# Performance work log

Hardware: AMD Instinct MI355X
Metric: run time of the kernel (lower is better)

## Reference

```python
import jax, jax.numpy as jnp
import numpy as np

LAMBDA_COLOR = 0.01
BLUR = 0.01          # geomloss blur
P = 2                # geomloss p
EPS_FINAL = BLUR ** P  # 1e-4
# Note: with scaling=1.2 (>1), geomloss's epsilon_schedule arange is empty, so
# eps_list = [diameter**p, blur**p] -> exactly two annealing stages.


def cost_matrix(x, y, lambda_color):
    # x: [B,N,6], y: [B,M,6]
    cx, col_x = x[..., :3], x[..., 3:]
    cy, col_y = y[..., :3], y[..., 3:]
    max_norm = jnp.max(jnp.linalg.norm(jnp.concatenate([cx, cy], axis=1), axis=-1))
    s = 1.0 / (max_norm + 1e-6)
    cxn, cyn = cx * s, cy * s
    coord = jnp.sum((cxn[:, :, None, :] - cyn[:, None, :, :]) ** 2, axis=-1)  # [B,N,M]
    col_x = jnp.clip(col_x, 0.0, 1.0)
    col_y = jnp.clip(col_y, 0.0, 1.0)
    col = jnp.sum((col_x[:, :, None, :] - col_y[:, None, :, :]) ** 2, axis=-1)
    return jnp.maximum(coord + lambda_color * col, 0.0)


def softmin(eps, C, h):
    # h: [B,M] = log_weights + potential/eps ; C: [B,N,M]
    return -eps * jax.nn.logsumexp(h[:, None, :] - C / eps, axis=2)  # [B,N]


def sinkhorn_distance(x, y, lambda_color):
    B, N, _ = x.shape
    M = y.shape[1]
    a_log = jnp.full((B, N), -np.log(N), dtype=x.dtype)
    b_log = jnp.full((B, M), -np.log(M), dtype=x.dtype)

    C_xy = cost_matrix(x, y, lambda_color)          # [B,N,M]
    C_yx = jnp.swapaxes(C_xy, 1, 2)                 # cost is symmetric in x<->y

    # diameter over raw 6-d features (geomloss max_diameter)
    pts = jnp.concatenate([x.reshape(-1, x.shape[-1]), y.reshape(-1, y.shape[-1])], axis=0)
    diameter = jnp.linalg.norm(pts.max(0) - pts.min(0))
    eps_list = (diameter ** P, jnp.asarray(EPS_FINAL, x.dtype))

    # Sinkhorn loop runs without gradient through the potentials (geomloss semantics)
    Cs_xy = jax.lax.stop_gradient(C_xy)
    Cs_yx = jax.lax.stop_gradient(C_yx)

    eps = eps_list[0]
    f = softmin(eps, Cs_xy, b_log)   # potential on x
    g = softmin(eps, Cs_yx, a_log)   # potential on y
    for eps in eps_list:
        ft = softmin(eps, Cs_xy, b_log + g / eps)
        gt = softmin(eps, Cs_yx, a_log + f / eps)
        f, g = 0.5 * (f + ft), 0.5 * (g + gt)

    # final extrapolation with gradient-carrying cost, detached dual potentials
    eps = eps_list[-1]
    f_new = softmin(eps, C_xy, b_log + jax.lax.stop_gradient(g) / eps)
    g_new = softmin(eps, C_yx, a_log + jax.lax.stop_gradient(f) / eps)

    # <a,f> + <b,g> with uniform weights
    ot = f_new.mean(axis=1) + g_new.mean(axis=1)   # [B]
    return ot.mean() * 10.0


def setup_inputs() -> dict:
    key = jax.random.key(0)
    kx, ky = jax.random.split(key)
    x = jax.random.normal(kx, (4, 4096, 6), dtype=jnp.float32)
    y = jax.random.normal(ky, (4, 4096, 6), dtype=jnp.float32)
    return {"x": x, "y": y}


def reference(x, y):
    return sinkhorn_distance(x, y, LAMBDA_COLOR)
```

## Files before the change

### kernel.cpp

```cpp
#include <hip/hip_runtime.h>

#define ROWS 16384
#define PTS_TOTAL 32768
#define NSM_BLK 256

#define LOG2E 1.4426950408889634f
#define LN2   0.6931471805599453f
#define NEG_LOG2M (-12.0f)
#define EPS1LNM 8.317766166719343e-4f

typedef _Float16 h2 __attribute__((ext_vector_type(2)));
typedef _Float16 v8h __attribute__((ext_vector_type(8)));
typedef float f32x4 __attribute__((ext_vector_type(4)));

__device__ inline float fexp2(float x) { return __builtin_amdgcn_exp2f(x); }
__device__ inline float flog2(float x) { return __builtin_amdgcn_logf(x); }

__device__ inline unsigned fenc(float f) {
  unsigned u = __float_as_uint(f);
  return (u & 0x80000000u) ? ~u : (u | 0x80000000u);
}
__device__ inline float fdec(unsigned u) {
  return (u & 0x80000000u) ? __uint_as_float(u & 0x7fffffffu)
                           : __uint_as_float(~u);
}
__device__ inline unsigned pkh2(float a, float b) {
  h2 hv; hv.x = (_Float16)a; hv.y = (_Float16)b;
  return __builtin_bit_cast(unsigned, hv);
}
__device__ inline v8h bcv8(uint4 u) { return __builtin_bit_cast(v8h, u); }

__device__ inline float mkv(const float* __restrict__ p, float s, float* v) {
  v[0] = p[0] * s; v[1] = p[1] * s; v[2] = p[2] * s;
  v[3] = 0.1f * fminf(fmaxf(p[3], 0.0f), 1.0f);
  v[4] = 0.1f * fminf(fmaxf(p[4], 0.0f), 1.0f);
  v[5] = 0.1f * fminf(fmaxf(p[5], 0.0f), 1.0f);
  return v[0]*v[0] + v[1]*v[1] + v[2]*v[2] + v[3]*v[3] + v[4]*v[4] + v[5]*v[5];
}

__device__ inline float taylor_f(const float* __restrict__ M, const float* v,
                                 float q, float eps0) {
  float sc2 = 2.0f * LOG2E / eps0;
  float p[6];
#pragma unroll
  for (int d = 0; d < 6; ++d) p[d] = v[d] * sc2;
  float t1 = 0.0f;
#pragma unroll
  for (int d = 0; d < 6; ++d) t1 += p[d] * M[1 + d];
  float t2 = 0.0f;
  int kk = 7;
#pragma unroll
  for (int d = 0; d < 6; ++d) {
#pragma unroll
    for (int e = d; e < 6; ++e) {
      float coef = (d == e) ? 1.0f : 2.0f;
      t2 += coef * p[d] * p[e] * M[kk];
      kk++;
    }
  }
  float S = M[0] + LN2 * t1 + (0.5f * LN2 * LN2) * t2;
  return q - eps0 * LN2 * flog2(S);
}

__device__ inline void mom28(float* acc, float wgt, const float* v) {
  acc[0] = wgt;
  int kk = 1;
#pragma unroll
  for (int d = 0; d < 6; ++d) acc[kk++] = wgt * v[d];
#pragma unroll
  for (int d = 0; d < 6; ++d) {
    float wv = wgt * v[d];
#pragma unroll
    for (int e = d; e < 6; ++e) acc[kk++] = wv * v[e];
  }
}

__device__ inline void red28g(float* acc, float* __restrict__ dst,
                              float (*shf)[28], int t, int wave, int lane) {
#pragma unroll
  for (int off = 32; off > 0; off >>= 1) {
#pragma unroll
    for (int k = 0; k < 28; ++k) acc[k] += __shfl_xor(acc[k], off);
  }
  if (lane == 0) {
#pragma unroll
    for (int k = 0; k < 28; ++k) shf[wave][k] = acc[k];
  }
  __syncthreads();
  if (t < 28) dst[t] = (shf[0][t] + shf[1][t]) + (shf[2][t] + shf[3][t]);
}

__device__ inline void se_from_rmax(const unsigned* __restrict__ RMAXu,
                                    unsigned (*shu)[13], float& s, float& eps0,
                                    int t, int wave, int lane) {
  int set = t & 127;
  unsigned e[13];
#pragma unroll
  for (int k = 0; k < 13; ++k) e[k] = RMAXu[set * 16 + k];
#pragma unroll
  for (int off = 32; off > 0; off >>= 1) {
#pragma unroll
    for (int k = 0; k < 13; ++k) {
      unsigned o = (unsigned)__shfl_xor((int)e[k], off);
      e[k] = e[k] > o ? e[k] : o;
    }
  }
  if (lane == 0) {
#pragma unroll
    for (int k = 0; k < 13; ++k) shu[wave][k] = e[k];
  }
  __syncthreads();
  unsigned mm[13];
#pragma unroll
  for (int k = 0; k < 13; ++k) {
    unsigned v0 = shu[0][k] > shu[1][k] ? shu[0][k] : shu[1][k];
    unsigned v1 = shu[2][k] > shu[3][k] ? shu[2][k] : shu[3][k];
    mm[k] = v0 > v1 ? v0 : v1;
  }
  s = 1.0f / (sqrtf(fdec(mm[0])) + 1e-6f);
  eps0 = 0.0f;
#pragma unroll
  for (int k = 0; k < 6; ++k) {
    float dd = fdec(mm[1 + k]) + fdec(mm[7 + k]);
    eps0 += dd * dd;
  }
}

__global__ __launch_bounds__(256) void k1_max(
    const float* __restrict__ x, const float* __restrict__ y,
    float* __restrict__ w) {
  unsigned* BARC = (unsigned*)w;
  unsigned* RMAX = (unsigned*)w + 64;
  const int t = threadIdx.x, wave = t >> 6, lane = t & 63, bx = blockIdx.x;
  if (bx == 0 && t == 0) BARC[0] = 0u;
  const int g0 = bx * 256;
  bool isx = g0 < ROWS;
  __shared__ float4 st[384];
  const float4* src =
      (const float4*)((isx ? x : y) + (size_t)(g0 & (ROWS - 1)) * 6);
  st[t] = src[t];
  if (t < 128) st[256 + t] = src[256 + t];
  __syncthreads();
  const float* sp = (const float*)st + t * 6;
  float d[6];
#pragma unroll
  for (int k = 0; k < 6; ++k) d[k] = sp[k];
  unsigned e[13];
  e[0] = fenc(d[0] * d[0] + d[1] * d[1] + d[2] * d[2]);
#pragma unroll
  for (int k = 0; k < 6; ++k) {
    e[1 + k] = fenc(d[k]);
    e[7 + k] = fenc(-d[k]);
  }
#pragma unroll
  for (int off = 32; off > 0; off >>= 1) {
#pragma unroll
    for (int k = 0; k < 13; ++k) {
      unsigned o = (unsigned)__shfl_xor((int)e[k], off);
      e[k] = e[k] > o ? e[k] : o;
    }
  }
  __shared__ unsigned shu[4][13];
  if (lane == 0) {
#pragma unroll
    for (int k = 0; k < 13; ++k) shu[wave][k] = e[k];
  }
  __syncthreads();
  if (t < 13) {
    unsigned v = shu[0][t];
#pragma unroll
    for (int wv = 1; wv < 4; ++wv) v = v > shu[wv][t] ? v : shu[wv][t];
    RMAX[bx * 16 + t] = v;
  }
}

__global__ __launch_bounds__(256) void k2_pack(
    const float* __restrict__ x, const float* __restrict__ y,
    float* __restrict__ w) {
  const int t = threadIdx.x, wave = t >> 6, lane = t & 63, bx = blockIdx.x;
  const unsigned* RMAX = (const unsigned*)w + 64;
  float* MOMP1 = w + 2560;
  float* base = w + 16384;
  uint4* AREC = (uint4*)base;
  float* Qarr = base + 3 * 4 * PTS_TOTAL;

  __shared__ unsigned shu[4][13];
  __shared__ float shf[4][28];
  float s, eps0;
  se_from_rmax(RMAX, shu, s, eps0, t, wave, lane);

  const int g = bx * 256 + t;
  const int side = g >> 14;
  const float* p = (side ? y : x) + (size_t)(g & (ROWS - 1)) * 6;
  float v[6]; float q = mkv(p, s, v);
  Qarr[g] = q;
  unsigned w01 = pkh2(v[0], v[1]), w23 = pkh2(v[2], v[3]), w45 = pkh2(v[4], v[5]);
  AREC[g] = (uint4){w01, w23, w45, pkh2(1.0f, 0.0f)};

  float wgt = fexp2(NEG_LOG2M - q * (LOG2E / eps0));
  float acc[28];
  mom28(acc, wgt, v);
  red28g(acc, MOMP1 + (size_t)bx * 32, shf, t, wave, lane);
}

__global__ __launch_bounds__(256) void k3_rows1(
    const float* __restrict__ x, const float* __restrict__ y,
    float* __restrict__ w) {
  const int t = threadIdx.x, wave = t >> 6, lane = t & 63, bx = blockIdx.x;
  const unsigned* RMAX = (const unsigned*)w + 64;
  const float* MOMP1 = w + 2560;
  float* MOMP2 = w + 2560 + 4096;
  float* base = w + 16384;
  float* FG1 = base + 3 * 4 * PTS_TOTAL + PTS_TOTAL + PTS_TOTAL;

  __shared__ unsigned shu[4][13];
  __shared__ float shf[4][28];
  __shared__ float M1opp[28];
  float s, eps0;
  se_from_rmax(RMAX, shu, s, eps0, t, wave, lane);

  const int g = bx * 256 + t;
  const int side = g >> 14;
  const int batch = (g >> 12) & 3;
  if (t < 28) {
    const float* mp = MOMP1 + ((size_t)((side ^ 1) * 64 + batch * 16)) * 32 + t;
    float m = 0.0f;
#pragma unroll
    for (int j = 0; j < 16; ++j) m += mp[j * 32];
    M1opp[t] = m;
  }
  __syncthreads();

  const float* p = (side ? y : x) + (size_t)(g & (ROWS - 1)) * 6;
  float v[6]; float q = mkv(p, s, v);
  float f1 = taylor_f(M1opp, v, q, eps0);
  FG1[g] = f1;
  float w2 = fexp2(NEG_LOG2M + (f1 - q) * (LOG2E / eps0));
  float acc[28];
  mom28(acc, w2, v);
  red28g(acc, MOMP2 + (size_t)bx * 32, shf, t, wave, lane);
}

__global__ __launch_bounds__(256) void k4_rows2(
    const float* __restrict__ x, const float* __restrict__ y,
    float* __restrict__ w) {
  const int t = threadIdx.x, wave = t >> 6, lane = t & 63, bx = blockIdx.x;
  const unsigned* RMAX = (const unsigned*)w + 64;
  const float* MOMP2 = w + 2560 + 4096;
  float* base = w + 16384;
  uint4* BRECA = (uint4*)base + PTS_TOTAL;
  float* Qarr = base + 3 * 4 * PTS_TOTAL;
  float* FG2 = Qarr + PTS_TOTAL;
  const float* FG1 = FG2 + PTS_TOTAL;

  __shared__ unsigned shu[4][13];
  __shared__ float M2opp[28];
  float s, eps0;
  se_from_rmax(RMAX, shu, s, eps0, t, wave, lane);

  const int g = bx * 256 + t;
  const int side = g >> 14;
  const int batch = (g >> 12) & 3;
  if (t < 28) {
    const float* mp = MOMP2 + ((size_t)((side ^ 1) * 64 + batch * 16)) * 32 + t;
    float m = 0.0f;
#pragma unroll
    for (int j = 0; j < 16; ++j) m += mp[j * 32];
    M2opp[t] = m;
  }
  __syncthreads();

  const float* p = (side ? y : x) + (size_t)(g & (ROWS - 1)) * 6;
  float v[6]; float q = mkv(p, s, v);
  float f1 = FG1[g];
  float f_t = taylor_f(M2opp, v, q, eps0);
  float f2 = 0.5f * (f1 + f_t);
  FG2[g] = f2;
  float hs2 = 0.5f * (f2 - q - EPS1LNM);
  unsigned w01 = pkh2(v[0], v[1]), w23 = pkh2(v[2], v[3]), w45 = pkh2(v[4], v[5]);
  BRECA[g] = (uint4){w01, w23, w45, pkh2(hs2, 0.0f)};
}

__device__ inline int xcd_rowgrp(int bx) {
  return (bx & 7) * 32 + (bx >> 3);
}

__device__ inline float softmax_max128L(int grow0,
                                        const uint4* __restrict__ AREC,
                                        const uint4* __restrict__ BIN,
                                        uint4* __restrict__ Blds,
                                        float (*lm)[64]) {
  int t = threadIdx.x;
  int w = t >> 6, lane = t & 63;
  int l16 = lane & 15;
  bool ldq = lane < 16;
  int side = grow0 >> 14;
  int batch = (grow0 & (ROWS - 1)) >> 12;
  int panel0 = (side ^ 1) * ROWS + batch * 4096;

  const uint4* gsrc = BIN + panel0 + w * 512 + lane;
  uint4* ldst = Blds + w * 512 + lane;
  uint4 s0 = gsrc[0],   s1 = gsrc[64],  s2 = gsrc[128], s3 = gsrc[192];
  uint4 s4 = gsrc[256], s5 = gsrc[320], s6 = gsrc[384], s7 = gsrc[448];

  uint4 z4 = (uint4){0u, 0u, 0u, 0u};
  uint4 a0u = z4, a1u = z4, a2u = z4, a3u = z4;
  int arow = grow0 + (w >> 2) * 64;
  if (ldq) {
    a0u = AREC[arow + l16];
    a1u = AREC[arow + 16 + l16];
    a2u = AREC[arow + 32 + l16];
    a3u = AREC[arow + 48 + l16];
  }
  v8h a0 = bcv8(a0u), a1 = bcv8(a1u), a2 = bcv8(a2u), a3 = bcv8(a3u);

  ldst[0] = s0;   ldst[64] = s1;  ldst[128] = s2; ldst[192] = s3;
  ldst[256] = s4; ldst[320] = s5; ldst[384] = s6; ldst[448] = s7;
  __syncthreads();

  f32x4 m0 = {-3.0e38f, -3.0e38f, -3.0e38f, -3.0e38f};
  f32x4 m1 = m0, m2 = m0, m3 = m0;
  const f32x4 cz = {0.0f, 0.0f, 0.0f, 0.0f};
  const int colq = (w & 3) * 1024;

#pragma unroll 8
  for (int tt = 0; tt < 64; ++tt) {
    uint4 bu = z4;
    if (ldq) bu = Blds[colq + tt * 16 + l16];
    v8h b = bcv8(bu);
    f32x4 d0 = __builtin_amdgcn_mfma_f32_16x16x32_f16(a0, b, cz, 0, 0, 0);
    f32x4 d1 = __builtin_amdgcn_mfma_f32_16x16x32_f16(a1, b, cz, 0, 0, 0);
    f32x4 d2 = __builtin_amdgcn_mfma_f32_16x16x32_f16(a2, b, cz, 0, 0, 0);
    f32x4 d3 = __builtin_amdgcn_mfma_f32_16x16x32_f16(a3, b, cz, 0, 0, 0);
    m0 = __builtin_elementwise_max(m0, d0);
    m1 = __builtin_elementwise_max(m1, d1);
    m2 = __builtin_elementwise_max(m2, d2);
    m3 = __builtin_elementwise_max(m3, d3);
  }

#pragma unroll
  for (int off = 1; off <= 8; off <<= 1) {
#pragma unroll
    for (int r = 0; r < 4; ++r) {
      m0[r] = fmaxf(m0[r], __shfl_xor(m0[r], off));
      m1[r] = fmaxf(m1[r], __shfl_xor(m1[r], off));
      m2[r] = fmaxf(m2[r], __shfl_xor(m2[r], off));
      m3[r] = fmaxf(m3[r], __shfl_xor(m3[r], off));
    }
  }
  if (l16 == 0) {
    int qd = lane >> 4;
#pragma unroll
    for (int r = 0; r < 4; ++r) {
      lm[w][qd * 4 + r]      = m0[r];
      lm[w][16 + qd * 4 + r] = m1[r];
      lm[w][32 + qd * 4 + r] = m2[r];
      lm[w][48 + qd * 4 + r] = m3[r];
    }
  }
  __syncthreads();
  float m = 0.0f;
  if (t < 128) {
    int half4 = (t >> 6) * 4, lr = t & 63;
    m = fmaxf(fmaxf(lm[half4][lr], lm[half4 + 1][lr]),
              fmaxf(lm[half4 + 2][lr], lm[half4 + 3][lr]));
  }
  return m;
}

__global__ __launch_bounds__(512) void kb_sm1(
    const uint4* __restrict__ AREC, const uint4* __restrict__ BIN,
    uint4* __restrict__ BOUT, const float* __restrict__ Qarr,
    const float* __restrict__ FG2) {
  __shared__ uint4 Blds[4096];
  __shared__ float lm[8][64];
  int t = threadIdx.x;
  int grow0 = xcd_rowgrp(blockIdx.x) * 128;
  float qv = 0.0f, fprev = 0.0f;
  uint4 ar = (uint4){0u, 0u, 0u, 0u};
  if (t < 128) {
    int gg = grow0 + t;
    qv = Qarr[gg];
    fprev = FG2[gg];
    ar = AREC[gg];
  }
  float m = softmax_max128L(grow0, AREC, BIN, Blds, lm);
  if (t < 128) {
    float f_t = qv - 2.0f * m;
    float fo = 0.5f * (fprev + f_t);
    float hs = 0.5f * (fo - qv - EPS1LNM);
    BOUT[grow0 + t] = (uint4){ar.x, ar.y, ar.z, pkh2(hs, 0.0f)};
  }
}

__global__ __launch_bounds__(512) void kc_sm2(
    const uint4* __restrict__ AREC, const uint4* __restrict__ BIN,
    const float* __restrict__ Qarr, float* __restrict__ PART,
    unsigned* __restrict__ BARC, float* __restrict__ out) {
  __shared__ uint4 Blds[4096];
  __shared__ float lm[8][64];
  __shared__ float fsh[128];
  __shared__ float fred[8];
  __shared__ int lastf;
  int t = threadIdx.x;
  int wave = t >> 6, lane = t & 63;
  int grow0 = xcd_rowgrp(blockIdx.x) * 128;
  float qv = 0.0f;
  if (t < 128) qv = Qarr[grow0 + t];
  float m = softmax_max128L(grow0, AREC, BIN, Blds, lm);
  if (t < 128) fsh[t] = qv - 2.0f * m;
  __syncthreads();
  if (t == 0) {
    float ssum = 0.0f;
#pragma unroll
    for (int k = 0; k < 128; ++k) ssum += fsh[k];
    __hip_atomic_store(&PART[blockIdx.x], ssum, __ATOMIC_RELAXED,
                       __HIP_MEMORY_SCOPE_AGENT);
    unsigned old = __hip_atomic_fetch_add(BARC, 1u, __ATOMIC_ACQ_REL,
                                          __HIP_MEMORY_SCOPE_AGENT);
    lastf = (old == (unsigned)(NSM_BLK - 1)) ? 1 : 0;
  }
  __syncthreads();
  if (lastf) {
    float a = 0.0f;
    if (t < NSM_BLK)
      a = __hip_atomic_load(&PART[t], __ATOMIC_RELAXED,
                            __HIP_MEMORY_SCOPE_AGENT);
#pragma unroll
    for (int off = 32; off > 0; off >>= 1) a += __shfl_xor(a, off);
    if (lane == 0) fred[wave] = a;
    __syncthreads();
    if (t == 0) {
      float s8 = 0.0f;
#pragma unroll
      for (int k = 0; k < 8; ++k) s8 += fred[k];
      out[0] = s8 * (10.0f / (float)ROWS);
    }
  }
}

extern "C" void kernel_launch(void* const* d_in, const int* in_sizes, int n_in,
                              void* d_out, int out_size, void* d_ws,
                              size_t ws_size, hipStream_t stream) {
  const float* x = (const float*)d_in[0];
  const float* y = (const float*)d_in[1];
  float* out = (float*)d_out;
  float* w = (float*)d_ws;

  unsigned* BARC = (unsigned*)w;
  float* base = w + 16384;
  uint4* AREC  = (uint4*)base;
  uint4* BRECA = AREC + PTS_TOTAL;
  uint4* BRECB = BRECA + PTS_TOTAL;
  float* Qarr  = base + 3 * 4 * PTS_TOTAL;
  float* FG2   = Qarr + PTS_TOTAL;
  float* FG1   = FG2 + PTS_TOTAL;
  float* PART  = FG1 + PTS_TOTAL;

  (void)ws_size;
  k1_max<<<128, 256, 0, stream>>>(x, y, w);
  k2_pack<<<128, 256, 0, stream>>>(x, y, w);
  k3_rows1<<<128, 256, 0, stream>>>(x, y, w);
  k4_rows2<<<128, 256, 0, stream>>>(x, y, w);
  kb_sm1<<<NSM_BLK, 512, 0, stream>>>(AREC, BRECA, BRECB, Qarr, FG2);
  kc_sm2<<<NSM_BLK, 512, 0, stream>>>(AREC, BRECB, Qarr, PART, BARC, out);
}
```

Baseline: 97.81 us.

## Repartition softmin max so each wave covers all rows over its own column slice

Each wave now computes MFMA row maxima for all 128 rows against only the 512 columns it staged itself, instead of 64 rows against 1024 shared columns. Because a wave reads only LDS it wrote, the block-wide barrier after staging is replaced by a wave-local lgkmcnt wait. This halves LDS B reads per MFMA and removes a barrier, at the cost of holding eight A fragments and eight max accumulators per wave (more registers) and a larger cross-wave reduction buffer.

Measured after the change: 98.72 us. Within noise of the previous version (+0.9%).

```diff
diff --git a/kernel.cpp b/kernel.cpp
--- a/kernel.cpp
+++ b/kernel.cpp
@@ -285,11 +285,11 @@
   return (bx & 7) * 32 + (bx >> 3);
 }
 
-__device__ inline float softmax_max128L(int grow0,
-                                        const uint4* __restrict__ AREC,
-                                        const uint4* __restrict__ BIN,
-                                        uint4* __restrict__ Blds,
-                                        float (*lm)[64]) {
+__device__ inline float softmax_wp128(int grow0,
+                                      const uint4* __restrict__ AREC,
+                                      const uint4* __restrict__ BIN,
+                                      uint4* __restrict__ Blds,
+                                      float (*lm)[128]) {
   int t = threadIdx.x;
   int w = t >> 6, lane = t & 63;
   int l16 = lane & 15;
@@ -305,28 +305,29 @@
 
   uint4 z4 = (uint4){0u, 0u, 0u, 0u};
   uint4 a0u = z4, a1u = z4, a2u = z4, a3u = z4;
-  int arow = grow0 + (w >> 2) * 64;
+  uint4 a4u = z4, a5u = z4, a6u = z4, a7u = z4;
   if (ldq) {
-    a0u = AREC[arow + l16];
-    a1u = AREC[arow + 16 + l16];
-    a2u = AREC[arow + 32 + l16];
-    a3u = AREC[arow + 48 + l16];
+    a0u = AREC[grow0 + l16];        a1u = AREC[grow0 + 16 + l16];
+    a2u = AREC[grow0 + 32 + l16];   a3u = AREC[grow0 + 48 + l16];
+    a4u = AREC[grow0 + 64 + l16];   a5u = AREC[grow0 + 80 + l16];
+    a6u = AREC[grow0 + 96 + l16];   a7u = AREC[grow0 + 112 + l16];
   }
   v8h a0 = bcv8(a0u), a1 = bcv8(a1u), a2 = bcv8(a2u), a3 = bcv8(a3u);
+  v8h a4 = bcv8(a4u), a5 = bcv8(a5u), a6 = bcv8(a6u), a7 = bcv8(a7u);
 
   ldst[0] = s0;   ldst[64] = s1;  ldst[128] = s2; ldst[192] = s3;
   ldst[256] = s4; ldst[320] = s5; ldst[384] = s6; ldst[448] = s7;
-  __syncthreads();
+  asm volatile("s_waitcnt lgkmcnt(0)" ::: "memory");
 
   f32x4 m0 = {-3.0e38f, -3.0e38f, -3.0e38f, -3.0e38f};
-  f32x4 m1 = m0, m2 = m0, m3 = m0;
+  f32x4 m1 = m0, m2 = m0, m3 = m0, m4 = m0, m5 = m0, m6 = m0, m7 = m0;
   const f32x4 cz = {0.0f, 0.0f, 0.0f, 0.0f};
-  const int colq = (w & 3) * 1024;
-
-#pragma unroll 8
-  for (int tt = 0; tt < 64; ++tt) {
+  const int col0 = w * 512;
+
+#pragma unroll 4
+  for (int tt = 0; tt < 32; ++tt) {
     uint4 bu = z4;
-    if (ldq) bu = Blds[colq + tt * 16 + l16];
+    if (ldq) bu = Blds[col0 + tt * 16 + l16];
     v8h b = bcv8(bu);
     f32x4 d0 = __builtin_amdgcn_mfma_f32_16x16x32_f16(a0, b, cz, 0, 0, 0);
     f32x4 d1 = __builtin_amdgcn_mfma_f32_16x16x32_f16(a1, b, cz, 0, 0, 0);
@@ -336,6 +337,14 @@
     m1 = __builtin_elementwise_max(m1, d1);
     m2 = __builtin_elementwise_max(m2, d2);
     m3 = __builtin_elementwise_max(m3, d3);
+    f32x4 d4 = __builtin_amdgcn_mfma_f32_16x16x32_f16(a4, b, cz, 0, 0, 0);
+    f32x4 d5 = __builtin_amdgcn_mfma_f32_16x16x32_f16(a5, b, cz, 0, 0, 0);
+    f32x4 d6 = __builtin_amdgcn_mfma_f32_16x16x32_f16(a6, b, cz, 0, 0, 0);
+    f32x4 d7 = __builtin_amdgcn_mfma_f32_16x16x32_f16(a7, b, cz, 0, 0, 0);
+    m4 = __builtin_elementwise_max(m4, d4);
+    m5 = __builtin_elementwise_max(m5, d5);
+    m6 = __builtin_elementwise_max(m6, d6);
+    m7 = __builtin_elementwise_max(m7, d7);
   }
 
 #pragma unroll
@@ -346,24 +355,32 @@
       m1[r] = fmaxf(m1[r], __shfl_xor(m1[r], off));
       m2[r] = fmaxf(m2[r], __shfl_xor(m2[r], off));
       m3[r] = fmaxf(m3[r], __shfl_xor(m3[r], off));
+      m4[r] = fmaxf(m4[r], __shfl_xor(m4[r], off));
+      m5[r] = fmaxf(m5[r], __shfl_xor(m5[r], off));
+      m6[r] = fmaxf(m6[r], __shfl_xor(m6[r], off));
+      m7[r] = fmaxf(m7[r], __shfl_xor(m7[r], off));
     }
   }
   if (l16 == 0) {
     int qd = lane >> 4;
 #pragma unroll
     for (int r = 0; r < 4; ++r) {
-      lm[w][qd * 4 + r]      = m0[r];
-      lm[w][16 + qd * 4 + r] = m1[r];
-      lm[w][32 + qd * 4 + r] = m2[r];
-      lm[w][48 + qd * 4 + r] = m3[r];
+      lm[w][qd * 4 + r]       = m0[r];
+      lm[w][16 + qd * 4 + r]  = m1[r];
+      lm[w][32 + qd * 4 + r]  = m2[r];
+      lm[w][48 + qd * 4 + r]  = m3[r];
+      lm[w][64 + qd * 4 + r]  = m4[r];
+      lm[w][80 + qd * 4 + r]  = m5[r];
+      lm[w][96 + qd * 4 + r]  = m6[r];
+      lm[w][112 + qd * 4 + r] = m7[r];
     }
   }
   __syncthreads();
   float m = 0.0f;
   if (t < 128) {
-    int half4 = (t >> 6) * 4, lr = t & 63;
-    m = fmaxf(fmaxf(lm[half4][lr], lm[half4 + 1][lr]),
-              fmaxf(lm[half4 + 2][lr], lm[half4 + 3][lr]));
+    float ma = fmaxf(fmaxf(lm[0][t], lm[1][t]), fmaxf(lm[2][t], lm[3][t]));
+    float mb = fmaxf(fmaxf(lm[4][t], lm[5][t]), fmaxf(lm[6][t], lm[7][t]));
+    m = fmaxf(ma, mb);
   }
   return m;
 }
@@ -373,7 +390,7 @@
     uint4* __restrict__ BOUT, const float* __restrict__ Qarr,
     const float* __restrict__ FG2) {
   __shared__ uint4 Blds[4096];
-  __shared__ float lm[8][64];
+  __shared__ float lm[8][128];
   int t = threadIdx.x;
   int grow0 = xcd_rowgrp(blockIdx.x) * 128;
   float qv = 0.0f, fprev = 0.0f;
@@ -384,7 +401,7 @@
     fprev = FG2[gg];
     ar = AREC[gg];
   }
-  float m = softmax_max128L(grow0, AREC, BIN, Blds, lm);
+  float m = softmax_wp128(grow0, AREC, BIN, Blds, lm);
   if (t < 128) {
     float f_t = qv - 2.0f * m;
     float fo = 0.5f * (fprev + f_t);
@@ -398,7 +415,7 @@
     const float* __restrict__ Qarr, float* __restrict__ PART,
     unsigned* __restrict__ BARC, float* __restrict__ out) {
   __shared__ uint4 Blds[4096];
-  __shared__ float lm[8][64];
+  __shared__ float lm[8][128];
   __shared__ float fsh[128];
   __shared__ float fred[8];
   __shared__ int lastf;
@@ -407,7 +424,7 @@
   int grow0 = xcd_rowgrp(blockIdx.x) * 128;
   float qv = 0.0f;
   if (t < 128) qv = Qarr[grow0 + t];
-  float m = softmax_max128L(grow0, AREC, BIN, Blds, lm);
+  float m = softmax_wp128(grow0, AREC, BIN, Blds, lm);
   if (t < 128) fsh[t] = qv - 2.0f * m;
   __syncthreads();
   if (t == 0) {
```

## Fuse four prologue kernels into one persistent kernel with grid barriers

Applied to the files above, without the earlier changes.

Replaces the four small prologue kernels (max, pack, first and second Taylor-moment steps) with one 64-block, 512-thread kernel. The stages are separated by atomic-counter grid barriers, and each thread keeps its point data in registers across them. This removes three kernel launch gaps, the redundant global reductions that recomputed scale and eps in every kernel, and the FG1 round-trip through memory. A small init kernel zeroes the barrier counters. It relies on all 64 blocks being co-resident, and it trades launch overhead for spin-wait barrier latency.

Measured after the change: 102.4 us. 1.05x slower.

```diff
diff --git a/kernel.cpp b/kernel.cpp
--- a/kernel.cpp
+++ b/kernel.cpp
@@ -3,6 +3,7 @@
 #define ROWS 16384
 #define PTS_TOTAL 32768
 #define NSM_BLK 256
+#define NEPS_BLK 64
 
 #define LOG2E 1.4426950408889634f
 #define LN2   0.6931471805599453f
@@ -30,11 +31,11 @@
 }
 __device__ inline v8h bcv8(uint4 u) { return __builtin_bit_cast(v8h, u); }
 
-__device__ inline float mkv(const float* __restrict__ p, float s, float* v) {
-  v[0] = p[0] * s; v[1] = p[1] * s; v[2] = p[2] * s;
-  v[3] = 0.1f * fminf(fmaxf(p[3], 0.0f), 1.0f);
-  v[4] = 0.1f * fminf(fmaxf(p[4], 0.0f), 1.0f);
-  v[5] = 0.1f * fminf(fmaxf(p[5], 0.0f), 1.0f);
+__device__ inline float mkv_d(const float* d, float s, float* v) {
+  v[0] = d[0] * s; v[1] = d[1] * s; v[2] = d[2] * s;
+  v[3] = 0.1f * fminf(fmaxf(d[3], 0.0f), 1.0f);
+  v[4] = 0.1f * fminf(fmaxf(d[4], 0.0f), 1.0f);
+  v[5] = 0.1f * fminf(fmaxf(d[5], 0.0f), 1.0f);
   return v[0]*v[0] + v[1]*v[1] + v[2]*v[2] + v[3]*v[3] + v[4]*v[4] + v[5]*v[5];
 }
 
@@ -75,209 +76,189 @@
   }
 }
 
-__device__ inline void red28g(float* acc, float* __restrict__ dst,
-                              float (*shf)[28], int t, int wave, int lane) {
-#pragma unroll
-  for (int off = 32; off > 0; off >>= 1) {
-#pragma unroll
-    for (int k = 0; k < 28; ++k) acc[k] += __shfl_xor(acc[k], off);
-  }
-  if (lane == 0) {
-#pragma unroll
-    for (int k = 0; k < 28; ++k) shf[wave][k] = acc[k];
-  }
-  __syncthreads();
-  if (t < 28) dst[t] = (shf[0][t] + shf[1][t]) + (shf[2][t] + shf[3][t]);
-}
-
-__device__ inline void se_from_rmax(const unsigned* __restrict__ RMAXu,
-                                    unsigned (*shu)[13], float& s, float& eps0,
-                                    int t, int wave, int lane) {
-  int set = t & 127;
-  unsigned e[13];
-#pragma unroll
-  for (int k = 0; k < 13; ++k) e[k] = RMAXu[set * 16 + k];
-#pragma unroll
-  for (int off = 32; off > 0; off >>= 1) {
-#pragma unroll
-    for (int k = 0; k < 13; ++k) {
-      unsigned o = (unsigned)__shfl_xor((int)e[k], off);
-      e[k] = e[k] > o ? e[k] : o;
-    }
-  }
-  if (lane == 0) {
-#pragma unroll
-    for (int k = 0; k < 13; ++k) shu[wave][k] = e[k];
-  }
-  __syncthreads();
-  unsigned mm[13];
-#pragma unroll
-  for (int k = 0; k < 13; ++k) {
-    unsigned v0 = shu[0][k] > shu[1][k] ? shu[0][k] : shu[1][k];
-    unsigned v1 = shu[2][k] > shu[3][k] ? shu[2][k] : shu[3][k];
-    mm[k] = v0 > v1 ? v0 : v1;
-  }
-  s = 1.0f / (sqrtf(fdec(mm[0])) + 1e-6f);
-  eps0 = 0.0f;
-#pragma unroll
-  for (int k = 0; k < 6; ++k) {
-    float dd = fdec(mm[1 + k]) + fdec(mm[7 + k]);
-    eps0 += dd * dd;
-  }
-}
-
-__global__ __launch_bounds__(256) void k1_max(
-    const float* __restrict__ x, const float* __restrict__ y,
-    float* __restrict__ w) {
-  unsigned* BARC = (unsigned*)w;
-  unsigned* RMAX = (unsigned*)w + 64;
-  const int t = threadIdx.x, wave = t >> 6, lane = t & 63, bx = blockIdx.x;
-  if (bx == 0 && t == 0) BARC[0] = 0u;
-  const int g0 = bx * 256;
-  bool isx = g0 < ROWS;
-  __shared__ float4 st[384];
-  const float4* src =
-      (const float4*)((isx ? x : y) + (size_t)(g0 & (ROWS - 1)) * 6);
-  st[t] = src[t];
-  if (t < 128) st[256 + t] = src[256 + t];
-  __syncthreads();
-  const float* sp = (const float*)st + t * 6;
-  float d[6];
-#pragma unroll
-  for (int k = 0; k < 6; ++k) d[k] = sp[k];
-  unsigned e[13];
-  e[0] = fenc(d[0] * d[0] + d[1] * d[1] + d[2] * d[2]);
-#pragma unroll
-  for (int k = 0; k < 6; ++k) {
-    e[1 + k] = fenc(d[k]);
-    e[7 + k] = fenc(-d[k]);
-  }
-#pragma unroll
-  for (int off = 32; off > 0; off >>= 1) {
-#pragma unroll
-    for (int k = 0; k < 13; ++k) {
-      unsigned o = (unsigned)__shfl_xor((int)e[k], off);
-      e[k] = e[k] > o ? e[k] : o;
-    }
-  }
-  __shared__ unsigned shu[4][13];
-  if (lane == 0) {
-#pragma unroll
-    for (int k = 0; k < 13; ++k) shu[wave][k] = e[k];
-  }
-  __syncthreads();
-  if (t < 13) {
-    unsigned v = shu[0][t];
-#pragma unroll
-    for (int wv = 1; wv < 4; ++wv) v = v > shu[wv][t] ? v : shu[wv][t];
-    RMAX[bx * 16 + t] = v;
-  }
-}
-
-__global__ __launch_bounds__(256) void k2_pack(
+__device__ inline void gbar(unsigned* c, unsigned n) {
+  __syncthreads();
+  if (threadIdx.x == 0) {
+    __hip_atomic_fetch_add(c, 1u, __ATOMIC_ACQ_REL, __HIP_MEMORY_SCOPE_AGENT);
+    while (__hip_atomic_load(c, __ATOMIC_ACQUIRE, __HIP_MEMORY_SCOPE_AGENT) < n)
+      __builtin_amdgcn_s_sleep(2);
+  }
+  __syncthreads();
+}
+
+__global__ __launch_bounds__(64) void k0_init(float* __restrict__ w) {
+  if (threadIdx.x < 32) ((unsigned*)w)[threadIdx.x] = 0u;
+}
+
+__global__ __launch_bounds__(512) void keps(
     const float* __restrict__ x, const float* __restrict__ y,
     float* __restrict__ w) {
   const int t = threadIdx.x, wave = t >> 6, lane = t & 63, bx = blockIdx.x;
-  const unsigned* RMAX = (const unsigned*)w + 64;
+  unsigned* CNT = (unsigned*)w + 16;
+  unsigned* RMAX = (unsigned*)w + 64;
   float* MOMP1 = w + 2560;
+  float* MOMP2 = w + 2560 + 2048;
   float* base = w + 16384;
-  uint4* AREC = (uint4*)base;
-  float* Qarr = base + 3 * 4 * PTS_TOTAL;
-
-  __shared__ unsigned shu[4][13];
-  __shared__ float shf[4][28];
-  float s, eps0;
-  se_from_rmax(RMAX, shu, s, eps0, t, wave, lane);
-
-  const int g = bx * 256 + t;
-  const int side = g >> 14;
-  const float* p = (side ? y : x) + (size_t)(g & (ROWS - 1)) * 6;
-  float v[6]; float q = mkv(p, s, v);
+  uint4* AREC  = (uint4*)base;
+  uint4* BRECA = (uint4*)base + PTS_TOTAL;
+  float* Qarr  = base + 3 * 4 * PTS_TOTAL;
+  float* FG2   = Qarr + PTS_TOTAL;
+
+  const int g = bx * 512 + t;
+  const int side = bx >> 5;
+  const int batch = (g >> 12) & 3;
+
+  __shared__ float4 st[768];
+  __shared__ unsigned shu[8][13];
+  __shared__ float shf[8][28];
+  __shared__ float sse[2];
+  __shared__ float Msh[28];
+
+  const int g0l = (bx & 31) * 512;
+  const float4* src = (const float4*)((side ? y : x) + (size_t)g0l * 6);
+  st[t] = src[t];
+  if (t < 256) st[512 + t] = src[512 + t];
+  __syncthreads();
+  const float* sp = (const float*)st + t * 6;
+  float d[6];
+#pragma unroll
+  for (int k = 0; k < 6; ++k) d[k] = sp[k];
+  {
+    unsigned e[13];
+    e[0] = fenc(d[0] * d[0] + d[1] * d[1] + d[2] * d[2]);
+#pragma unroll
+    for (int k = 0; k < 6; ++k) {
+      e[1 + k] = fenc(d[k]);
+      e[7 + k] = fenc(-d[k]);
+    }
+#pragma unroll
+    for (int off = 32; off > 0; off >>= 1) {
+#pragma unroll
+      for (int k = 0; k < 13; ++k) {
+        unsigned o = (unsigned)__shfl_xor((int)e[k], off);
+        e[k] = e[k] > o ? e[k] : o;
+      }
+    }
+    if (lane == 0) {
+#pragma unroll
+      for (int k = 0; k < 13; ++k) shu[wave][k] = e[k];
+    }
+    __syncthreads();
+    if (t < 13) {
+      unsigned v = shu[0][t];
+#pragma unroll
+      for (int wv = 1; wv < 8; ++wv) v = v > shu[wv][t] ? v : shu[wv][t];
+      __hip_atomic_store(&RMAX[bx * 16 + t], v, __ATOMIC_RELAXED,
+                         __HIP_MEMORY_SCOPE_AGENT);
+    }
+  }
+  gbar(CNT + 0, NEPS_BLK);
+
+  if (t < 64) {
+    unsigned e[13];
+#pragma unroll
+    for (int k = 0; k < 13; ++k)
+      e[k] = __hip_atomic_load(&RMAX[t * 16 + k], __ATOMIC_RELAXED,
+                               __HIP_MEMORY_SCOPE_AGENT);
+#pragma unroll
+    for (int off = 32; off > 0; off >>= 1) {
+#pragma unroll
+      for (int k = 0; k < 13; ++k) {
+        unsigned o = (unsigned)__shfl_xor((int)e[k], off);
+        e[k] = e[k] > o ? e[k] : o;
+      }
+    }
+    if (t == 0) {
+      float s_ = 1.0f / (sqrtf(fdec(e[0])) + 1e-6f);
+      float e0 = 0.0f;
+#pragma unroll
+      for (int k = 0; k < 6; ++k) {
+        float dd = fdec(e[1 + k]) + fdec(e[7 + k]);
+        e0 += dd * dd;
+      }
+      sse[0] = s_; sse[1] = e0;
+    }
+  }
+  __syncthreads();
+  const float s = sse[0], eps0 = sse[1];
+
+  float v[6];
+  float q = mkv_d(d, s, v);
   Qarr[g] = q;
   unsigned w01 = pkh2(v[0], v[1]), w23 = pkh2(v[2], v[3]), w45 = pkh2(v[4], v[5]);
   AREC[g] = (uint4){w01, w23, w45, pkh2(1.0f, 0.0f)};
-
-  float wgt = fexp2(NEG_LOG2M - q * (LOG2E / eps0));
-  float acc[28];
-  mom28(acc, wgt, v);
-  red28g(acc, MOMP1 + (size_t)bx * 32, shf, t, wave, lane);
-}
-
-__global__ __launch_bounds__(256) void k3_rows1(
-    const float* __restrict__ x, const float* __restrict__ y,
-    float* __restrict__ w) {
-  const int t = threadIdx.x, wave = t >> 6, lane = t & 63, bx = blockIdx.x;
-  const unsigned* RMAX = (const unsigned*)w + 64;
-  const float* MOMP1 = w + 2560;
-  float* MOMP2 = w + 2560 + 4096;
-  float* base = w + 16384;
-  float* FG1 = base + 3 * 4 * PTS_TOTAL + PTS_TOTAL + PTS_TOTAL;
-
-  __shared__ unsigned shu[4][13];
-  __shared__ float shf[4][28];
-  __shared__ float M1opp[28];
-  float s, eps0;
-  se_from_rmax(RMAX, shu, s, eps0, t, wave, lane);
-
-  const int g = bx * 256 + t;
-  const int side = g >> 14;
-  const int batch = (g >> 12) & 3;
+  {
+    float wgt = fexp2(NEG_LOG2M - q * (LOG2E / eps0));
+    float acc[28];
+    mom28(acc, wgt, v);
+#pragma unroll
+    for (int off = 32; off > 0; off >>= 1) {
+#pragma unroll
+      for (int k = 0; k < 28; ++k) acc[k] += __shfl_xor(acc[k], off);
+    }
+    if (lane == 0) {
+#pragma unroll
+      for (int k = 0; k < 28; ++k) shf[wave][k] = acc[k];
+    }
+    __syncthreads();
+    if (t < 28) {
+      float vv = 0.0f;
+#pragma unroll
+      for (int wv = 0; wv < 8; ++wv) vv += shf[wv][t];
+      __hip_atomic_store(&MOMP1[bx * 32 + t], vv, __ATOMIC_RELAXED,
+                         __HIP_MEMORY_SCOPE_AGENT);
+    }
+  }
+  gbar(CNT + 1, NEPS_BLK);
+
+  const int obase = (side ^ 1) * 32 + batch * 8;
   if (t < 28) {
-    const float* mp = MOMP1 + ((size_t)((side ^ 1) * 64 + batch * 16)) * 32 + t;
     float m = 0.0f;
 #pragma unroll
-    for (int j = 0; j < 16; ++j) m += mp[j * 32];
-    M1opp[t] = m;
-  }
-  __syncthreads();
-
-  const float* p = (side ? y : x) + (size_t)(g & (ROWS - 1)) * 6;
-  float v[6]; float q = mkv(p, s, v);
-  float f1 = taylor_f(M1opp, v, q, eps0);
-  FG1[g] = f1;
-  float w2 = fexp2(NEG_LOG2M + (f1 - q) * (LOG2E / eps0));
-  float acc[28];
-  mom28(acc, w2, v);
-  red28g(acc, MOMP2 + (size_t)bx * 32, shf, t, wave, lane);
-}
-
-__global__ __launch_bounds__(256) void k4_rows2(
-    const float* __restrict__ x, const float* __restrict__ y,
-    float* __restrict__ w) {
-  const int t = threadIdx.x, wave = t >> 6, lane = t & 63, bx = blockIdx.x;
-  const unsigned* RMAX = (const unsigned*)w + 64;
-  const float* MOMP2 = w + 2560 + 4096;
-  float* base = w + 16384;
-  uint4* BRECA = (uint4*)base + PTS_TOTAL;
-  float* Qarr = base + 3 * 4 * PTS_TOTAL;
-  float* FG2 = Qarr + PTS_TOTAL;
-  const float* FG1 = FG2 + PTS_TOTAL;
-
-  __shared__ unsigned shu[4][13];
-  __shared__ float M2opp[28];
-  float s, eps0;
-  se_from_rmax(RMAX, shu, s, eps0, t, wave, lane);
-
-  const int g = bx * 256 + t;
-  const int side = g >> 14;
-  const int batch = (g >> 12) & 3;
+    for (int j = 0; j < 8; ++j)
+      m += __hip_atomic_load(&MOMP1[(obase + j) * 32 + t], __ATOMIC_RELAXED,
+                             __HIP_MEMORY_SCOPE_AGENT);
+    Msh[t] = m;
+  }
+  __syncthreads();
+  float f1 = taylor_f(Msh, v, q, eps0);
+  {
+    float w2 = fexp2(NEG_LOG2M + (f1 - q) * (LOG2E / eps0));
+    float acc[28];
+    mom28(acc, w2, v);
+#pragma unroll
+    for (int off = 32; off > 0; off >>= 1) {
+#pragma unroll
+      for (int k = 0; k < 28; ++k) acc[k] += __shfl_xor(acc[k], off);
+    }
+    if (lane == 0) {
+#pragma unroll
+      for (int k = 0; k < 28; ++k) shf[wave][k] = acc[k];
+    }
+    __syncthreads();
+    if (t < 28) {
+      float vv = 0.0f;
+#pragma unroll
+      for (int wv = 0; wv < 8; ++wv) vv += shf[wv][t];
+      __hip_atomic_store(&MOMP2[bx * 32 + t], vv, __ATOMIC_RELAXED,
+                         __HIP_MEMORY_SCOPE_AGENT);
+    }
+  }
+  gbar(CNT + 2, NEPS_BLK);
+
   if (t < 28) {
-    const float* mp = MOMP2 + ((size_t)((side ^ 1) * 64 + batch * 16)) * 32 + t;
     float m = 0.0f;
 #pragma unroll
-    for (int j = 0; j < 16; ++j) m += mp[j * 32];
-    M2opp[t] = m;
-  }
-  __syncthreads();
-
-  const float* p = (side ? y : x) + (size_t)(g & (ROWS - 1)) * 6;
-  float v[6]; float q = mkv(p, s, v);
-  float f1 = FG1[g];
-  float f_t = taylor_f(M2opp, v, q, eps0);
+    for (int j = 0; j < 8; ++j)
+      m += __hip_atomic_load(&MOMP2[(obase + j) * 32 + t], __ATOMIC_RELAXED,
+                             __HIP_MEMORY_SCOPE_AGENT);
+    Msh[t] = m;
+  }
+  __syncthreads();
+  float f_t = taylor_f(Msh, v, q, eps0);
   float f2 = 0.5f * (f1 + f_t);
   FG2[g] = f2;
   float hs2 = 0.5f * (f2 - q - EPS1LNM);
-  unsigned w01 = pkh2(v[0], v[1]), w23 = pkh2(v[2], v[3]), w45 = pkh2(v[4], v[5]);
   BRECA[g] = (uint4){w01, w23, w45, pkh2(hs2, 0.0f)};
 }
 
@@ -454,14 +435,11 @@
   uint4* BRECB = BRECA + PTS_TOTAL;
   float* Qarr  = base + 3 * 4 * PTS_TOTAL;
   float* FG2   = Qarr + PTS_TOTAL;
-  float* FG1   = FG2 + PTS_TOTAL;
-  float* PART  = FG1 + PTS_TOTAL;
+  float* PART  = FG2 + PTS_TOTAL;
 
   (void)ws_size;
-  k1_max<<<128, 256, 0, stream>>>(x, y, w);
-  k2_pack<<<128, 256, 0, stream>>>(x, y, w);
-  k3_rows1<<<128, 256, 0, stream>>>(x, y, w);
-  k4_rows2<<<128, 256, 0, stream>>>(x, y, w);
+  k0_init<<<1, 64, 0, stream>>>(w);
+  keps<<<NEPS_BLK, 512, 0, stream>>>(x, y, w);
   kb_sm1<<<NSM_BLK, 512, 0, stream>>>(AREC, BRECA, BRECB, Qarr, FG2);
   kc_sm2<<<NSM_BLK, 512, 0, stream>>>(AREC, BRECB, Qarr, PART, BARC, out);
 }
```
